# Performance work log

Measured on AMD Instinct MI355X. Metric: run time of the kernel, lower is better.

## Reference

```python
import jax, jax.numpy as jnp
import numpy as np

B, IN_DIM, HID, OUT_DIM = 32768, 784, 256, 1000
L, CURV = 3, 1e-3
LOG2_H = 8  # log2(HID)
EPS_BN = 1e-5

def _layer_param_sizes():
    return [(HID // (2 * (1 << (l % LOG2_H)))) * 2 for l in range(L)]

def setup_inputs():
    key = jax.random.key(0)
    ks = jax.random.split(key, 4)
    total = sum(_layer_param_sizes())  # 448
    return {
        "x": jax.random.normal(ks[0], (B, IN_DIM), jnp.float32),
        "fc1_w": jax.random.normal(ks[1], (HID, IN_DIM), jnp.float32) / np.sqrt(IN_DIM).astype(np.float32),
        "fc1_b": jnp.zeros((HID,), jnp.float32),
        "bn1_gamma": jnp.ones((HID,), jnp.float32),
        "bn1_beta": jnp.zeros((HID,), jnp.float32),
        "bf_params": jax.random.normal(ks[2], (total,), jnp.float32) * 0.01,
        "bn2_gamma": jnp.ones((HID,), jnp.float32),
        "bn2_beta": jnp.zeros((HID,), jnp.float32),
        "fc2_w": jax.random.normal(ks[3], (OUT_DIM, HID), jnp.float32) / np.sqrt(HID).astype(np.float32),
        "fc2_b": jnp.zeros((OUT_DIM,), jnp.float32),
    }

def _batchnorm(h, gamma, beta):
    # training-mode BatchNorm1d: batch mean / biased variance
    mu = jnp.mean(h, axis=0)
    var = jnp.mean(jnp.square(h - mu), axis=0)
    return gamma * (h - mu) * jax.lax.rsqrt(var + EPS_BN) + beta

def _log_map0(x, c):
    # Poincare ball log map at origin: artanh(sqrt(c)|x|) * x / (sqrt(c)|x|)
    sn = jnp.sqrt(c) * jnp.linalg.norm(x, axis=-1, keepdims=True)
    sn = jnp.clip(sn, 1e-7, 1.0 - 1e-6)
    return (jnp.arctanh(sn) / sn) * x

def _exp_map0(u, c):
    sn = jnp.maximum(jnp.sqrt(c) * jnp.linalg.norm(u, axis=-1, keepdims=True), 1e-7)
    return (jnp.tanh(sn) / sn) * u

def _hyper_butterfly(h, params, c):
    u = _log_map0(h, c)
    off = 0
    for l in range(L):
        bs = 1 << (l % LOG2_H)      # half-block size at stage l
        nb = HID // (2 * bs)        # number of 2x2-rotation blocks
        p = params[off:off + 2 * nb]
        a = p[:nb][None, :, None]   # [1, nb, 1]
        b = p[nb:][None, :, None]
        v = u.reshape(-1, nb, 2, bs)
        x1, x2 = v[:, :, 0], v[:, :, 1]
        y1 = a * x1 + b * x2
        y2 = -b * x1 + a * x2
        u = jnp.stack([y1, y2], axis=2).reshape(-1, HID)
        off += 2 * nb
    return _exp_map0(u, c)

def reference(x, fc1_w, fc1_b, bn1_gamma, bn1_beta, bf_params, bn2_gamma, bn2_beta, fc2_w, fc2_b):
    h = x @ fc1_w.T + fc1_b
    h = jax.nn.relu(_batchnorm(h, bn1_gamma, bn1_beta))
    ht = _hyper_butterfly(h, bf_params, CURV)
    ht = jax.nn.relu(_batchnorm(ht, bn2_gamma, bn2_beta))
    return ht @ fc2_w.T + fc2_b
```

## Files before the change

kernel.cpp:

```cpp
#include <hip/hip_runtime.h>
#include <math.h>

#define NBATCH 32768
#define IND    784
#define KPAD1  800
#define HIDD   256
#define OUTD   1000
#define OUTDP  1024

typedef _Float16 half8  __attribute__((ext_vector_type(8)));
typedef _Float16 half4v __attribute__((ext_vector_type(4)));
typedef float    floatx4 __attribute__((ext_vector_type(4)));

#define GAS __attribute__((address_space(1)))
#define LAS __attribute__((address_space(3)))

#define WAITVM_BAR(N)                                                      \
    asm volatile("s_waitcnt vmcnt(" #N ") lgkmcnt(0)" ::: "memory");       \
    __builtin_amdgcn_s_barrier();                                          \
    __builtin_amdgcn_sched_barrier(0)

__device__ __forceinline__ void gld16(const void* g, void* l) {
    __builtin_amdgcn_global_load_lds((const GAS void*)g, (LAS void*)l, 16, 0, 0);
}

__device__ __forceinline__ float wave_allreduce_sum(float v) {
    #pragma unroll
    for (int off = 32; off >= 1; off >>= 1) v += __shfl_xor(v, off);
    return v;
}

__global__ __launch_bounds__(256)
void prep_kernel(const float* __restrict__ w1, _Float16* __restrict__ w1h,
                 const float* __restrict__ w2, _Float16* __restrict__ w2h,
                 float* __restrict__ stat)
{
    const int tid = threadIdx.x;
    if (blockIdx.x == 0) {
        for (int j = tid; j < 1024 + 16; j += 256) stat[j] = 0.0f;
    }
    const int NW1 = HIDD * (KPAD1 / 8);
    const int NW2 = OUTDP * (HIDD / 8);
    for (int i = blockIdx.x * 256 + tid; i < NW1 + NW2; i += (int)gridDim.x * 256) {
        half8 o;
        if (i < NW1) {
            const int r = i / (KPAD1 / 8), c8 = (i % (KPAD1 / 8)) * 8;
            if (c8 + 8 <= IND) {
                const float* s = &w1[(size_t)r * IND + c8];
                float4 v0 = *(const float4*)s, v1 = *(const float4*)(s + 4);
                o[0]=(_Float16)v0.x; o[1]=(_Float16)v0.y; o[2]=(_Float16)v0.z; o[3]=(_Float16)v0.w;
                o[4]=(_Float16)v1.x; o[5]=(_Float16)v1.y; o[6]=(_Float16)v1.z; o[7]=(_Float16)v1.w;
            } else {
                #pragma unroll
                for (int j = 0; j < 8; ++j) o[j] = (_Float16)0.0f;
            }
            *(half8*)&w1h[(size_t)r * KPAD1 + c8] = o;
        } else {
            const int k = i - NW1;
            const int r = k >> 5, c8 = (k & 31) * 8;
            if (r < OUTD) {
                const float* s = &w2[(size_t)r * HIDD + c8];
                float4 v0 = *(const float4*)s, v1 = *(const float4*)(s + 4);
                o[0]=(_Float16)v0.x; o[1]=(_Float16)v0.y; o[2]=(_Float16)v0.z; o[3]=(_Float16)v0.w;
                o[4]=(_Float16)v1.x; o[5]=(_Float16)v1.y; o[6]=(_Float16)v1.z; o[7]=(_Float16)v1.w;
            } else {
                #pragma unroll
                for (int j = 0; j < 8; ++j) o[j] = (_Float16)0.0f;
            }
            *(half8*)&w2h[(size_t)r * HIDD + c8] = o;
        }
    }
}

__global__ __launch_bounds__(256, 2)
void gemm1_kernel(const float* __restrict__ x, const _Float16* __restrict__ w1h,
                  const float* __restrict__ b1, const float* __restrict__ zbuf,
                  float* __restrict__ h, float* __restrict__ sum1, float* __restrict__ ssq1)
{
    __shared__ __align__(16) float    ldsA[3][4096];
    __shared__ __align__(16) _Float16 ldsB[3][4096];
    __shared__ float redS[2][128], redQ[2][128];

    const int tid  = threadIdx.x;
    const int bid0 = blockIdx.x;
    const int vbid = (bid0 & 7) * 64 + (bid0 >> 3);
    const int bm = vbid >> 1, bn = vbid & 1;
    const int m0 = bm * 128, n0 = bn * 128;
    const int lane = tid & 63, wv = tid >> 6;
    const int wr = wv >> 1, wc = wv & 1;
    const int l15 = lane & 15, lg = lane >> 4;
    const int e7 = l15 & 7, e3 = l15 & 3;
    const int nt = KPAD1 / 32;

    const int arow = lane >> 3, agp = (lane & 7) ^ arow;
    const int brow = lane >> 2, bgp = (lane & 3) ^ (brow & 3);
    const float*    Ab = x   + (size_t)(m0 + arow) * IND   + agp * 4;
    const _Float16* Bb = w1h + (size_t)(n0 + brow) * KPAD1 + bgp * 8;

    floatx4 acc[4][4];
    #pragma unroll
    for (int i = 0; i < 4; ++i)
        #pragma unroll
        for (int j = 0; j < 4; ++j) acc[i][j] = (floatx4){0.f, 0.f, 0.f, 0.f};

    auto STAGE = [&](int buf, int t) {
        const int t32 = t * 32;
        const bool tok = t < nt;
        const bool aok = tok && (t32 + agp * 4) < IND;
        #pragma unroll
        for (int c = 0; c < 4; ++c) {
            const int ch = wv + c * 4;
            const float* s = aok ? (Ab + (size_t)ch * 8 * IND + t32) : zbuf;
            gld16(s, &ldsA[buf][ch * 256]);
        }
        #pragma unroll
        for (int c = 0; c < 2; ++c) {
            const int ch = wv + c * 4;
            const void* s = tok ? (const void*)(Bb + (size_t)ch * 16 * KPAD1 + t32)
                                : (const void*)zbuf;
            gld16(s, &ldsB[buf][ch * 512]);
        }
    };

    STAGE(0, 0);
    STAGE(1, 1);
    WAITVM_BAR(6);

    int buf = 0;
    for (int t = 0; t < nt; ++t) {
        int nbuf = buf + 2; if (nbuf >= 3) nbuf -= 3;
        STAGE(nbuf, t + 2);
        half8 af[4], bfr[4];
        #pragma unroll
        for (int i = 0; i < 4; ++i) {
            const int rc = wr * 8 + i * 2 + (l15 >> 3);
            const float* base = &ldsA[buf][rc * 256 + e7 * 32];
            float4 va = *(const float4*)(base + (((2 * lg)     ^ e7) * 4));
            float4 vb = *(const float4*)(base + (((2 * lg + 1) ^ e7) * 4));
            half8 hv;
            hv[0]=(_Float16)va.x; hv[1]=(_Float16)va.y; hv[2]=(_Float16)va.z; hv[3]=(_Float16)va.w;
            hv[4]=(_Float16)vb.x; hv[5]=(_Float16)vb.y; hv[6]=(_Float16)vb.z; hv[7]=(_Float16)vb.w;
            af[i] = hv;
        }
        #pragma unroll
        for (int j = 0; j < 4; ++j)
            bfr[j] = *(const half8*)&ldsB[buf][(wc * 4 + j) * 512 + l15 * 32 + ((lg ^ e3) * 8)];
        #pragma unroll
        for (int i = 0; i < 4; ++i)
            #pragma unroll
            for (int j = 0; j < 4; ++j)
                acc[i][j] = __builtin_amdgcn_mfma_f32_16x16x32_f16(bfr[j], af[i], acc[i][j], 0, 0, 0);
        WAITVM_BAR(6);
        buf = (buf + 1 == 3) ? 0 : buf + 1;
    }

    float sJ[4][4], qJ[4][4];
    #pragma unroll
    for (int j = 0; j < 4; ++j)
        #pragma unroll
        for (int r = 0; r < 4; ++r) { sJ[j][r] = 0.f; qJ[j][r] = 0.f; }
    #pragma unroll
    for (int i = 0; i < 4; ++i) {
        const int m = m0 + wr * 64 + i * 16 + l15;
        #pragma unroll
        for (int j = 0; j < 4; ++j) {
            const int nb = n0 + wc * 64 + j * 16 + lg * 4;
            float4 bt = *reinterpret_cast<const float4*>(&b1[nb]);
            float v[4] = {acc[i][j][0] + bt.x, acc[i][j][1] + bt.y,
                          acc[i][j][2] + bt.z, acc[i][j][3] + bt.w};
            *reinterpret_cast<float4*>(&h[(size_t)m * HIDD + nb]) =
                make_float4(v[0], v[1], v[2], v[3]);
            #pragma unroll
            for (int r = 0; r < 4; ++r) { sJ[j][r] += v[r]; qJ[j][r] += v[r] * v[r]; }
        }
    }
    #pragma unroll
    for (int j = 0; j < 4; ++j)
        #pragma unroll
        for (int r = 0; r < 4; ++r) {
            float s = sJ[j][r], q = qJ[j][r];
            s += __shfl_xor(s, 1); s += __shfl_xor(s, 2);
            s += __shfl_xor(s, 4); s += __shfl_xor(s, 8);
            q += __shfl_xor(q, 1); q += __shfl_xor(q, 2);
            q += __shfl_xor(q, 4); q += __shfl_xor(q, 8);
            if (l15 == 0) {
                redS[wr][wc * 64 + j * 16 + lg * 4 + r] = s;
                redQ[wr][wc * 64 + j * 16 + lg * 4 + r] = q;
            }
        }
    __syncthreads();
    if (tid < 128) {
        atomicAdd(&sum1[n0 + tid], redS[0][tid] + redS[1][tid]);
        atomicAdd(&ssq1[n0 + tid], redQ[0][tid] + redQ[1][tid]);
    }
}

__global__ __launch_bounds__(256)
void mid_kernel(const float* __restrict__ h, const float* __restrict__ bfp,
                const float* __restrict__ sum1, const float* __restrict__ ssq1,
                const float* __restrict__ g1, const float* __restrict__ be1,
                _Float16* __restrict__ ht16, float* __restrict__ sum2, float* __restrict__ ssq2)
{
    __shared__ float s1sh[256], t1sh[256];
    __shared__ float bsum[4][256], bssq[4][256];
    const int tid  = threadIdx.x;
    {
        const float inv = 1.0f / (float)NBATCH;
        const float mu  = sum1[tid] * inv;
        const float var = fmaxf(ssq1[tid] * inv - mu * mu, 0.0f);
        const float rs  = 1.0f / sqrtf(var + 1e-5f);
        const float sj  = g1[tid] * rs;
        s1sh[tid] = sj;
        t1sh[tid] = fmaf(-mu, sj, be1[tid]);
    }
    __syncthreads();

    const int w    = tid >> 6;
    const int lane = tid & 63;
    const int row0 = blockIdx.x * 64 + w * 16;
    const int c0   = lane * 4;

    const float4 s1v = *reinterpret_cast<const float4*>(&s1sh[c0]);
    const float4 t1v = *reinterpret_cast<const float4*>(&t1sh[c0]);
    const float a0 = bfp[2 * lane],       a1 = bfp[2 * lane + 1];
    const float b0 = bfp[128 + 2 * lane], b1 = bfp[128 + 2 * lane + 1];
    const float a2 = bfp[256 + lane],     b2 = bfp[320 + lane];
    const float a3 = bfp[384 + (lane >> 1)], b3 = bfp[416 + (lane >> 1)];
    const float sgn = (lane & 1) ? -1.0f : 1.0f;
    const float sc  = sqrtf(1e-3f);

    float ps0 = 0, ps1 = 0, ps2 = 0, ps3 = 0;
    float q0 = 0, q1 = 0, q2 = 0, q3 = 0;

    for (int r = 0; r < 16; ++r) {
        const int row = row0 + r;
        const float4 v = *reinterpret_cast<const float4*>(&h[(size_t)row * HIDD + c0]);
        float x0 = fmaxf(fmaf(v.x, s1v.x, t1v.x), 0.0f);
        float x1 = fmaxf(fmaf(v.y, s1v.y, t1v.y), 0.0f);
        float x2 = fmaxf(fmaf(v.z, s1v.z, t1v.z), 0.0f);
        float x3 = fmaxf(fmaf(v.w, s1v.w, t1v.w), 0.0f);
        float n2 = x0 * x0 + x1 * x1 + x2 * x2 + x3 * x3;
        n2 = wave_allreduce_sum(n2);
        float sn = sc * sqrtf(n2);
        sn = fminf(fmaxf(sn, 1e-7f), 1.0f - 1e-6f);
        const float ls = atanhf(sn) / sn;
        x0 *= ls; x1 *= ls; x2 *= ls; x3 *= ls;
        const float y0 = fmaf(a0, x0,  b0 * x1);
        const float y1 = fmaf(a0, x1, -b0 * x0);
        const float y2 = fmaf(a1, x2,  b1 * x3);
        const float y3 = fmaf(a1, x3, -b1 * x2);
        const float z0 = fmaf(a2, y0,  b2 * y2);
        const float z1 = fmaf(a2, y1,  b2 * y3);
        const float z2 = fmaf(a2, y2, -b2 * y0);
        const float z3 = fmaf(a2, y3, -b2 * y1);
        const float p0 = __shfl_xor(z0, 1);
        const float p1 = __shfl_xor(z1, 1);
        const float p2 = __shfl_xor(z2, 1);
        const float p3 = __shfl_xor(z3, 1);
        const float w0 = fmaf(a3, z0, sgn * (b3 * p0));
        const float w1 = fmaf(a3, z1, sgn * (b3 * p1));
        const float w2 = fmaf(a3, z2, sgn * (b3 * p2));
        const float w3 = fmaf(a3, z3, sgn * (b3 * p3));
        float m2 = w0 * w0 + w1 * w1 + w2 * w2 + w3 * w3;
        m2 = wave_allreduce_sum(m2);
        const float sn2 = fmaxf(sc * sqrtf(m2), 1e-7f);
        const float es = tanhf(sn2) / sn2;
        const float o0 = es * w0, o1 = es * w1, o2 = es * w2, o3 = es * w3;
        half4v hv;
        hv[0] = (_Float16)(o0 * 65536.0f); hv[1] = (_Float16)(o1 * 65536.0f);
        hv[2] = (_Float16)(o2 * 65536.0f); hv[3] = (_Float16)(o3 * 65536.0f);
        *reinterpret_cast<half4v*>(&ht16[(size_t)row * HIDD + c0]) = hv;
        ps0 += o0; ps1 += o1; ps2 += o2; ps3 += o3;
        q0 += o0 * o0; q1 += o1 * o1; q2 += o2 * o2; q3 += o3 * o3;
    }

    bsum[w][c0 + 0] = ps0; bsum[w][c0 + 1] = ps1; bsum[w][c0 + 2] = ps2; bsum[w][c0 + 3] = ps3;
    bssq[w][c0 + 0] = q0;  bssq[w][c0 + 1] = q1;  bssq[w][c0 + 2] = q2;  bssq[w][c0 + 3] = q3;
    __syncthreads();
    if (tid < 256) {
        const float s = bsum[0][tid] + bsum[1][tid] + bsum[2][tid] + bsum[3][tid];
        const float q = bssq[0][tid] + bssq[1][tid] + bssq[2][tid] + bssq[3][tid];
        atomicAdd(&sum2[tid], s);
        atomicAdd(&ssq2[tid], q);
    }
}

__global__ __launch_bounds__(256, 3)
void gemm2_kernel(const _Float16* __restrict__ ht16, const _Float16* __restrict__ w2h,
                  const float* __restrict__ b2,
                  const float* __restrict__ sum2, const float* __restrict__ ssq2,
                  const float* __restrict__ g2, const float* __restrict__ be2,
                  const float* __restrict__ zbuf, float* __restrict__ out)
{
    __shared__ __align__(16) _Float16 ldsA[3][4096];
    __shared__ __align__(16) _Float16 ldsB[3][4096];
    __shared__ float sf[256], tf[256];

    const int tid = threadIdx.x;
    {
        const float inv = 1.0f / (float)NBATCH;
        const float mu  = sum2[tid] * inv;
        const float var = fmaxf(ssq2[tid] * inv - mu * mu, 0.0f);
        const float rs  = 1.0f / sqrtf(var + 1e-5f);
        const float sj  = g2[tid] * rs;
        sf[tid] = sj * (1024.0f / 65536.0f);
        tf[tid] = fmaf(-mu, sj, be2[tid]) * 1024.0f;
    }

    const int bid0 = blockIdx.x;
    const int vbid = (bid0 & 7) * 256 + (bid0 >> 3);
    const int bm = vbid >> 3, bn = vbid & 7;
    const int m0 = bm * 128, n0 = bn * 128;
    const int lane = tid & 63, wv = tid >> 6;
    const int wr = wv >> 1, wc = wv & 1;
    const int l15 = lane & 15, lg = lane >> 4;
    const int e3 = l15 & 3;
    const int nt = HIDD / 32;

    const int srow = lane >> 2, sgp = (lane & 3) ^ (srow & 3);
    const _Float16* Ab = ht16 + (size_t)(m0 + srow) * HIDD + sgp * 8;
    const _Float16* Bb = w2h  + (size_t)(n0 + srow) * HIDD + sgp * 8;

    floatx4 acc[4][4];
    #pragma unroll
    for (int i = 0; i < 4; ++i)
        #pragma unroll
        for (int j = 0; j < 4; ++j) acc[i][j] = (floatx4){0.f, 0.f, 0.f, 0.f};

    auto STAGE = [&](int buf, int t) {
        const int t32 = t * 32;
        const bool tok = t < nt;
        #pragma unroll
        for (int c = 0; c < 2; ++c) {
            const int ch = wv + c * 4;
            const void* sa = tok ? (const void*)(Ab + (size_t)ch * 16 * HIDD + t32)
                                 : (const void*)zbuf;
            const void* sb = tok ? (const void*)(Bb + (size_t)ch * 16 * HIDD + t32)
                                 : (const void*)zbuf;
            gld16(sa, &ldsA[buf][ch * 512]);
            gld16(sb, &ldsB[buf][ch * 512]);
        }
    };

    STAGE(0, 0);
    STAGE(1, 1);
    WAITVM_BAR(4);

    int buf = 0;
    for (int t = 0; t < nt; ++t) {
        int nbuf = buf + 2; if (nbuf >= 3) nbuf -= 3;
        STAGE(nbuf, t + 2);
        const int kb = t * 32 + lg * 8;
        float4 s0 = *(const float4*)&sf[kb], s1 = *(const float4*)&sf[kb + 4];
        float4 t0 = *(const float4*)&tf[kb], t1 = *(const float4*)&tf[kb + 4];
        half8 af[4], bfr[4];
        #pragma unroll
        for (int i = 0; i < 4; ++i) {
            half8 v = *(const half8*)&ldsA[buf][(wr * 4 + i) * 512 + l15 * 32 + ((lg ^ e3) * 8)];
            half8 hv;
            hv[0] = (_Float16)fmaxf(fmaf((float)v[0], s0.x, t0.x), 0.0f);
            hv[1] = (_Float16)fmaxf(fmaf((float)v[1], s0.y, t0.y), 0.0f);
            hv[2] = (_Float16)fmaxf(fmaf((float)v[2], s0.z, t0.z), 0.0f);
            hv[3] = (_Float16)fmaxf(fmaf((float)v[3], s0.w, t0.w), 0.0f);
            hv[4] = (_Float16)fmaxf(fmaf((float)v[4], s1.x, t1.x), 0.0f);
            hv[5] = (_Float16)fmaxf(fmaf((float)v[5], s1.y, t1.y), 0.0f);
            hv[6] = (_Float16)fmaxf(fmaf((float)v[6], s1.z, t1.z), 0.0f);
            hv[7] = (_Float16)fmaxf(fmaf((float)v[7], s1.w, t1.w), 0.0f);
            af[i] = hv;
        }
        #pragma unroll
        for (int j = 0; j < 4; ++j)
            bfr[j] = *(const half8*)&ldsB[buf][(wc * 4 + j) * 512 + l15 * 32 + ((lg ^ e3) * 8)];
        #pragma unroll
        for (int i = 0; i < 4; ++i)
            #pragma unroll
            for (int j = 0; j < 4; ++j)
                acc[i][j] = __builtin_amdgcn_mfma_f32_16x16x32_f16(bfr[j], af[i], acc[i][j], 0, 0, 0);
        WAITVM_BAR(4);
        buf = (buf + 1 == 3) ? 0 : buf + 1;
    }
    asm volatile("s_waitcnt vmcnt(0)" ::: "memory");

    const float invScale = 1.0f / 1024.0f;
    #pragma unroll
    for (int i = 0; i < 4; ++i) {
        const int m = m0 + wr * 64 + i * 16 + l15;
        #pragma unroll
        for (int j = 0; j < 4; ++j) {
            const int nb = n0 + wc * 64 + j * 16 + lg * 4;
            float bj[4];
            if (nb + 4 <= OUTD) {
                float4 bt = *reinterpret_cast<const float4*>(&b2[nb]);
                bj[0] = bt.x; bj[1] = bt.y; bj[2] = bt.z; bj[3] = bt.w;
            } else {
                #pragma unroll
                for (int r = 0; r < 4; ++r) bj[r] = (nb + r < OUTD) ? b2[nb + r] : 0.0f;
            }
            float v[4];
            #pragma unroll
            for (int r = 0; r < 4; ++r) v[r] = fmaf(acc[i][j][r], invScale, bj[r]);
            if (nb + 4 <= OUTD) {
                *reinterpret_cast<float4*>(&out[(size_t)m * OUTD + nb]) =
                    make_float4(v[0], v[1], v[2], v[3]);
            } else {
                #pragma unroll
                for (int r = 0; r < 4; ++r)
                    if (nb + r < OUTD) out[(size_t)m * OUTD + nb + r] = v[r];
            }
        }
    }
}

extern "C" void kernel_launch(void* const* d_in, const int* in_sizes, int n_in,
                              void* d_out, int out_size, void* d_ws, size_t ws_size,
                              hipStream_t stream)
{
    const float* x   = (const float*)d_in[0];
    const float* w1  = (const float*)d_in[1];
    const float* b1  = (const float*)d_in[2];
    const float* g1  = (const float*)d_in[3];
    const float* be1 = (const float*)d_in[4];
    const float* bfp = (const float*)d_in[5];
    const float* g2  = (const float*)d_in[6];
    const float* be2 = (const float*)d_in[7];
    const float* w2  = (const float*)d_in[8];
    const float* b2  = (const float*)d_in[9];

    float* out = (float*)d_out;
    char*  wsb = (char*)d_ws;

    _Float16* ht16 = (_Float16*)(wsb);
    _Float16* w1h  = (_Float16*)(wsb + 16777216);
    _Float16* w2h  = (_Float16*)(wsb + 17186816);
    float*    stat = (float*)  (wsb + 17711104);
    float* sum1 = stat;
    float* ssq1 = stat + 256;
    float* sum2 = stat + 512;
    float* ssq2 = stat + 768;
    float* zbuf = stat + 1024;

    float* h = out;

    prep_kernel<<<232, 256, 0, stream>>>(w1, w1h, w2, w2h, stat);
    gemm1_kernel<<<512, 256, 0, stream>>>(x, w1h, b1, zbuf, h, sum1, ssq1);
    mid_kernel<<<512, 256, 0, stream>>>(h, bfp, sum1, ssq1, g1, be1, ht16, sum2, ssq2);
    gemm2_kernel<<<2048, 256, 0, stream>>>(ht16, w2h, b2, sum2, ssq2, g2, be2, zbuf, out);
}
```

Before: 129.4 us.

## Stage gemm1 A tiles via registers as fp16 to cut LDS and raise occupancy

The first GEMM now loads x tiles from global memory into registers, converts them to fp16, and writes them to a double-buffered fp16 LDS buffer. Previously it DMA'd fp32 data straight into a triple-buffered LDS area and converted on every fragment read. This halves LDS use for A, which allows launch bounds of three blocks per CU instead of two, and removes repeated conversions on the read side. In exchange it adds register pressure for the staged loads, a more complex two-phase unrolled loop with explicit vmcnt waits, and global-load latency that must be hidden by the register prefetch.

```diff
diff --git a/kernel.cpp b/kernel.cpp
--- a/kernel.cpp
+++ b/kernel.cpp
@@ -15,6 +15,7 @@
 #define GAS __attribute__((address_space(1)))
 #define LAS __attribute__((address_space(3)))
 
+#define WAITVM(N) asm volatile("s_waitcnt vmcnt(" #N ")" ::: "memory")
 #define WAITVM_BAR(N)                                                      \
     asm volatile("s_waitcnt vmcnt(" #N ") lgkmcnt(0)" ::: "memory");       \
     __builtin_amdgcn_s_barrier();                                          \
@@ -72,12 +73,12 @@
     }
 }
 
-__global__ __launch_bounds__(256, 2)
+__global__ __launch_bounds__(256, 3)
 void gemm1_kernel(const float* __restrict__ x, const _Float16* __restrict__ w1h,
                   const float* __restrict__ b1, const float* __restrict__ zbuf,
                   float* __restrict__ h, float* __restrict__ sum1, float* __restrict__ ssq1)
 {
-    __shared__ __align__(16) float    ldsA[3][4096];
+    __shared__ __align__(16) _Float16 ldsA[2][4096];
     __shared__ __align__(16) _Float16 ldsB[3][4096];
     __shared__ float redS[2][128], redQ[2][128];
 
@@ -89,12 +90,18 @@
     const int lane = tid & 63, wv = tid >> 6;
     const int wr = wv >> 1, wc = wv & 1;
     const int l15 = lane & 15, lg = lane >> 4;
-    const int e7 = l15 & 7, e3 = l15 & 3;
+    const int e3 = l15 & 3;
     const int nt = KPAD1 / 32;
 
-    const int arow = lane >> 3, agp = (lane & 7) ^ arow;
+    const int r0g = tid >> 2;
+    const int r1g = 64 + (tid >> 2);
+    const int kq  = tid & 3;
+    const int wpos0 = r0g * 32 + ((kq ^ (r0g & 3)) * 8);
+    const int wpos1 = r1g * 32 + ((kq ^ (r1g & 3)) * 8);
+    const float* Ab0 = x + (size_t)(m0 + r0g) * IND + kq * 8;
+    const float* Ab1 = x + (size_t)(m0 + r1g) * IND + kq * 8;
+
     const int brow = lane >> 2, bgp = (lane & 3) ^ (brow & 3);
-    const float*    Ab = x   + (size_t)(m0 + arow) * IND   + agp * 4;
     const _Float16* Bb = w1h + (size_t)(n0 + brow) * KPAD1 + bgp * 8;
 
     floatx4 acc[4][4];
@@ -103,56 +110,84 @@
         #pragma unroll
         for (int j = 0; j < 4; ++j) acc[i][j] = (floatx4){0.f, 0.f, 0.f, 0.f};
 
-    auto STAGE = [&](int buf, int t) {
+    floatx4 rgaE[4], rgaO[4];
+
+    auto A_ISSUE = [&](floatx4 (&rg)[4], int t) {
+        const int t32 = t * 32;
+        const bool v = (t32 + kq * 8) < IND;
+        const float* p0 = v ? (Ab0 + t32) : zbuf;
+        const float* p1 = v ? (Ab1 + t32) : zbuf;
+        rg[0] = *(const floatx4*)p0;
+        rg[1] = *(const floatx4*)(p0 + 4);
+        rg[2] = *(const floatx4*)p1;
+        rg[3] = *(const floatx4*)(p1 + 4);
+    };
+    auto A_WRITE = [&](floatx4 (&rg)[4], int wb) {
+        half8 h0, h1;
+        #pragma unroll
+        for (int j = 0; j < 4; ++j) {
+            h0[j] = (_Float16)rg[0][j]; h0[4 + j] = (_Float16)rg[1][j];
+            h1[j] = (_Float16)rg[2][j]; h1[4 + j] = (_Float16)rg[3][j];
+        }
+        *(half8*)&ldsA[wb][wpos0] = h0;
+        *(half8*)&ldsA[wb][wpos1] = h1;
+    };
+    auto B_ISSUE = [&](int bb, int t) {
         const int t32 = t * 32;
         const bool tok = t < nt;
-        const bool aok = tok && (t32 + agp * 4) < IND;
-        #pragma unroll
-        for (int c = 0; c < 4; ++c) {
-            const int ch = wv + c * 4;
-            const float* s = aok ? (Ab + (size_t)ch * 8 * IND + t32) : zbuf;
-            gld16(s, &ldsA[buf][ch * 256]);
-        }
         #pragma unroll
         for (int c = 0; c < 2; ++c) {
             const int ch = wv + c * 4;
             const void* s = tok ? (const void*)(Bb + (size_t)ch * 16 * KPAD1 + t32)
                                 : (const void*)zbuf;
-            gld16(s, &ldsB[buf][ch * 512]);
+            gld16(s, &ldsB[bb][ch * 512]);
         }
     };
 
-    STAGE(0, 0);
-    STAGE(1, 1);
-    WAITVM_BAR(6);
-
-    int buf = 0;
-    for (int t = 0; t < nt; ++t) {
-        int nbuf = buf + 2; if (nbuf >= 3) nbuf -= 3;
-        STAGE(nbuf, t + 2);
+    auto COMPUTE = [&](int abuf, int brd) {
         half8 af[4], bfr[4];
         #pragma unroll
-        for (int i = 0; i < 4; ++i) {
-            const int rc = wr * 8 + i * 2 + (l15 >> 3);
-            const float* base = &ldsA[buf][rc * 256 + e7 * 32];
-            float4 va = *(const float4*)(base + (((2 * lg)     ^ e7) * 4));
-            float4 vb = *(const float4*)(base + (((2 * lg + 1) ^ e7) * 4));
-            half8 hv;
-            hv[0]=(_Float16)va.x; hv[1]=(_Float16)va.y; hv[2]=(_Float16)va.z; hv[3]=(_Float16)va.w;
-            hv[4]=(_Float16)vb.x; hv[5]=(_Float16)vb.y; hv[6]=(_Float16)vb.z; hv[7]=(_Float16)vb.w;
-            af[i] = hv;
-        }
+        for (int i = 0; i < 4; ++i)
+            af[i] = *(const half8*)&ldsA[abuf][(wr * 64 + i * 16 + l15) * 32 + ((lg ^ e3) * 8)];
         #pragma unroll
         for (int j = 0; j < 4; ++j)
-            bfr[j] = *(const half8*)&ldsB[buf][(wc * 4 + j) * 512 + l15 * 32 + ((lg ^ e3) * 8)];
+            bfr[j] = *(const half8*)&ldsB[brd][(wc * 4 + j) * 512 + l15 * 32 + ((lg ^ e3) * 8)];
         #pragma unroll
         for (int i = 0; i < 4; ++i)
             #pragma unroll
             for (int j = 0; j < 4; ++j)
                 acc[i][j] = __builtin_amdgcn_mfma_f32_16x16x32_f16(bfr[j], af[i], acc[i][j], 0, 0, 0);
+    };
+
+    A_ISSUE(rgaE, 0); B_ISSUE(0, 0);
+    WAITVM(2);
+    A_WRITE(rgaE, 0);
+    A_ISSUE(rgaO, 1); B_ISSUE(1, 1);
+    WAITVM_BAR(6);
+
+    int b0 = 0;
+    for (int p = 0; p < 12; ++p) {
+        const int t  = p * 2;
+        const int b1v = b0 + 1 == 3 ? 0 : b0 + 1;
+        const int b2v = b1v + 1 == 3 ? 0 : b1v + 1;
+        A_ISSUE(rgaE, t + 2);
+        B_ISSUE(b2v, t + 2);
+        COMPUTE(0, b0);
+        __builtin_amdgcn_sched_barrier(0);
+        WAITVM(6);
+        A_WRITE(rgaO, 1);
         WAITVM_BAR(6);
-        buf = (buf + 1 == 3) ? 0 : buf + 1;
-    }
+        A_ISSUE(rgaO, t + 3);
+        B_ISSUE(b0, t + 3);
+        COMPUTE(1, b1v);
+        __builtin_amdgcn_sched_barrier(0);
+        WAITVM(6);
+        A_WRITE(rgaE, 0);
+        WAITVM_BAR(6);
+        b0 = b2v;
+    }
+    COMPUTE(0, b0);
+    WAITVM(0);
 
     float sJ[4][4], qJ[4][4];
     #pragma unroll
@@ -379,7 +414,7 @@
         WAITVM_BAR(4);
         buf = (buf + 1 == 3) ? 0 : buf + 1;
     }
-    asm volatile("s_waitcnt vmcnt(0)" ::: "memory");
+    WAITVM(0);
 
     const float invScale = 1.0f / 1024.0f;
     #pragma unroll
```

Result: faster. 126.4 us (-2.3%).

## Restructure gemm1 to full-N tiles with register-direct A loads

Applied to the files above, without the earlier changes.

gemm1 now has each 512-thread block compute a 128x256 tile, i.e. all of N, so each row of x is read once instead of twice. The A operand is loaded straight from global memory into registers per wave, bypassing LDS, while B is staged through LDS in five phases of 160 K. The aim is to halve x traffic and drop the A LDS round trip. The cost is more registers (16 accumulators plus 5 staged A fragments), 256 blocks at one block per CU, and coarser phase barriers with less overlap between loads and MFMA.

```diff
diff --git a/kernel.cpp b/kernel.cpp
--- a/kernel.cpp
+++ b/kernel.cpp
@@ -15,8 +15,13 @@
 #define GAS __attribute__((address_space(1)))
 #define LAS __attribute__((address_space(3)))
 
+#define WAITVM(N) asm volatile("s_waitcnt vmcnt(" #N ")" ::: "memory")
 #define WAITVM_BAR(N)                                                      \
     asm volatile("s_waitcnt vmcnt(" #N ") lgkmcnt(0)" ::: "memory");       \
+    __builtin_amdgcn_s_barrier();                                          \
+    __builtin_amdgcn_sched_barrier(0)
+#define LGKM_BAR                                                           \
+    asm volatile("s_waitcnt lgkmcnt(0)" ::: "memory");                     \
     __builtin_amdgcn_s_barrier();                                          \
     __builtin_amdgcn_sched_barrier(0)
 
@@ -72,126 +77,98 @@
     }
 }
 
-__global__ __launch_bounds__(256, 2)
+__global__ __launch_bounds__(512, 1)
 void gemm1_kernel(const float* __restrict__ x, const _Float16* __restrict__ w1h,
                   const float* __restrict__ b1, const float* __restrict__ zbuf,
                   float* __restrict__ h, float* __restrict__ sum1, float* __restrict__ ssq1)
 {
-    __shared__ __align__(16) float    ldsA[3][4096];
-    __shared__ __align__(16) _Float16 ldsB[3][4096];
-    __shared__ float redS[2][128], redQ[2][128];
+    __shared__ __align__(16) _Float16 ldsB[5][16][512];
+    __shared__ float redS[8][256], redQ[8][256];
 
     const int tid  = threadIdx.x;
-    const int bid0 = blockIdx.x;
-    const int vbid = (bid0 & 7) * 64 + (bid0 >> 3);
-    const int bm = vbid >> 1, bn = vbid & 1;
-    const int m0 = bm * 128, n0 = bn * 128;
-    const int lane = tid & 63, wv = tid >> 6;
-    const int wr = wv >> 1, wc = wv & 1;
-    const int l15 = lane & 15, lg = lane >> 4;
-    const int e7 = l15 & 7, e3 = l15 & 3;
-    const int nt = KPAD1 / 32;
-
-    const int arow = lane >> 3, agp = (lane & 7) ^ arow;
-    const int brow = lane >> 2, bgp = (lane & 3) ^ (brow & 3);
-    const float*    Ab = x   + (size_t)(m0 + arow) * IND   + agp * 4;
-    const _Float16* Bb = w1h + (size_t)(n0 + brow) * KPAD1 + bgp * 8;
-
-    floatx4 acc[4][4];
-    #pragma unroll
-    for (int i = 0; i < 4; ++i)
-        #pragma unroll
-        for (int j = 0; j < 4; ++j) acc[i][j] = (floatx4){0.f, 0.f, 0.f, 0.f};
-
-    auto STAGE = [&](int buf, int t) {
-        const int t32 = t * 32;
-        const bool tok = t < nt;
-        const bool aok = tok && (t32 + agp * 4) < IND;
-        #pragma unroll
-        for (int c = 0; c < 4; ++c) {
-            const int ch = wv + c * 4;
-            const float* s = aok ? (Ab + (size_t)ch * 8 * IND + t32) : zbuf;
-            gld16(s, &ldsA[buf][ch * 256]);
-        }
-        #pragma unroll
-        for (int c = 0; c < 2; ++c) {
-            const int ch = wv + c * 4;
-            const void* s = tok ? (const void*)(Bb + (size_t)ch * 16 * KPAD1 + t32)
-                                : (const void*)zbuf;
-            gld16(s, &ldsB[buf][ch * 512]);
-        }
+    const int w    = tid >> 6;
+    const int lane = tid & 63;
+    const int l15  = lane & 15, lg = lane >> 4;
+    const int m0   = (int)blockIdx.x * 128;
+    const int mrow = m0 + w * 16 + l15;
+
+    const int bri = lane >> 2;
+    const int bgp = (lane & 3) ^ (bri & 3);
+    const float* aptr = x + (size_t)mrow * IND;
+
+    floatx4 acc[16];
+    #pragma unroll
+    for (int j = 0; j < 16; ++j) acc[j] = (floatx4){0.f, 0.f, 0.f, 0.f};
+
+    floatx4 a0[2], a1[2], a2[2], a3[2], a4[2];
+
+    auto A_ISSUE = [&](floatx4 (&st)[2], int kt) {
+        const int col = kt * 32 + lg * 8;
+        const float* p = (col < IND) ? (aptr + col) : zbuf;
+        st[0] = *(const floatx4*)p;
+        st[1] = *(const floatx4*)(p + 4);
     };
-
-    STAGE(0, 0);
-    STAGE(1, 1);
-    WAITVM_BAR(6);
-
-    int buf = 0;
-    for (int t = 0; t < nt; ++t) {
-        int nbuf = buf + 2; if (nbuf >= 3) nbuf -= 3;
-        STAGE(nbuf, t + 2);
-        half8 af[4], bfr[4];
-        #pragma unroll
-        for (int i = 0; i < 4; ++i) {
-            const int rc = wr * 8 + i * 2 + (l15 >> 3);
-            const float* base = &ldsA[buf][rc * 256 + e7 * 32];
-            float4 va = *(const float4*)(base + (((2 * lg)     ^ e7) * 4));
-            float4 vb = *(const float4*)(base + (((2 * lg + 1) ^ e7) * 4));
-            half8 hv;
-            hv[0]=(_Float16)va.x; hv[1]=(_Float16)va.y; hv[2]=(_Float16)va.z; hv[3]=(_Float16)va.w;
-            hv[4]=(_Float16)vb.x; hv[5]=(_Float16)vb.y; hv[6]=(_Float16)vb.z; hv[7]=(_Float16)vb.w;
-            af[i] = hv;
-        }
-        #pragma unroll
-        for (int j = 0; j < 4; ++j)
-            bfr[j] = *(const half8*)&ldsB[buf][(wc * 4 + j) * 512 + l15 * 32 + ((lg ^ e3) * 8)];
-        #pragma unroll
-        for (int i = 0; i < 4; ++i)
+    auto B_STAGE = [&](int p) {
+        #pragma unroll
+        for (int ks = 0; ks < 5; ++ks)
             #pragma unroll
-            for (int j = 0; j < 4; ++j)
-                acc[i][j] = __builtin_amdgcn_mfma_f32_16x16x32_f16(bfr[j], af[i], acc[i][j], 0, 0, 0);
-        WAITVM_BAR(6);
-        buf = (buf + 1 == 3) ? 0 : buf + 1;
-    }
-
-    float sJ[4][4], qJ[4][4];
-    #pragma unroll
-    for (int j = 0; j < 4; ++j)
-        #pragma unroll
-        for (int r = 0; r < 4; ++r) { sJ[j][r] = 0.f; qJ[j][r] = 0.f; }
-    #pragma unroll
-    for (int i = 0; i < 4; ++i) {
-        const int m = m0 + wr * 64 + i * 16 + l15;
-        #pragma unroll
-        for (int j = 0; j < 4; ++j) {
-            const int nb = n0 + wc * 64 + j * 16 + lg * 4;
-            float4 bt = *reinterpret_cast<const float4*>(&b1[nb]);
-            float v[4] = {acc[i][j][0] + bt.x, acc[i][j][1] + bt.y,
-                          acc[i][j][2] + bt.z, acc[i][j][3] + bt.w};
-            *reinterpret_cast<float4*>(&h[(size_t)m * HIDD + nb]) =
-                make_float4(v[0], v[1], v[2], v[3]);
-            #pragma unroll
-            for (int r = 0; r < 4; ++r) { sJ[j][r] += v[r]; qJ[j][r] += v[r] * v[r]; }
-        }
-    }
-    #pragma unroll
-    for (int j = 0; j < 4; ++j)
+            for (int c = 0; c < 2; ++c) {
+                const int ch = w * 2 + c;
+                const _Float16* src = w1h + (size_t)(ch * 16 + bri) * KPAD1
+                                      + p * 160 + ks * 32 + bgp * 8;
+                gld16(src, &ldsB[ks][ch][lane * 8]);
+            }
+    };
+    auto STEP = [&](floatx4 (&st)[2], int ks) {
+        half8 af;
+        #pragma unroll
+        for (int q = 0; q < 4; ++q) { af[q] = (_Float16)st[0][q]; af[4+q] = (_Float16)st[1][q]; }
+        const int ro = l15 * 32 + ((lg ^ (l15 & 3)) * 8);
+        #pragma unroll
+        for (int j = 0; j < 16; ++j) {
+            half8 bf = *(const half8*)&ldsB[ks][j][ro];
+            acc[j] = __builtin_amdgcn_mfma_f32_16x16x32_f16(bf, af, acc[j], 0, 0, 0);
+        }
+    };
+
+    #pragma unroll
+    for (int p = 0; p < 5; ++p) {
+        if (p > 0) { LGKM_BAR; }
+        B_STAGE(p);
+        A_ISSUE(a0, 5*p+0); A_ISSUE(a1, 5*p+1); A_ISSUE(a2, 5*p+2);
+        A_ISSUE(a3, 5*p+3); A_ISSUE(a4, 5*p+4);
+        WAITVM_BAR(10);
+        STEP(a0, 0); STEP(a1, 1); STEP(a2, 2); STEP(a3, 3); STEP(a4, 4);
+    }
+
+    #pragma unroll
+    for (int j = 0; j < 16; ++j) {
+        const int nb = j * 16 + lg * 4;
+        float4 bt = *reinterpret_cast<const float4*>(&b1[nb]);
+        float v[4] = {acc[j][0] + bt.x, acc[j][1] + bt.y,
+                      acc[j][2] + bt.z, acc[j][3] + bt.w};
+        *reinterpret_cast<float4*>(&h[(size_t)mrow * HIDD + nb]) =
+            make_float4(v[0], v[1], v[2], v[3]);
         #pragma unroll
         for (int r = 0; r < 4; ++r) {
-            float s = sJ[j][r], q = qJ[j][r];
+            float s = v[r], q = v[r] * v[r];
             s += __shfl_xor(s, 1); s += __shfl_xor(s, 2);
             s += __shfl_xor(s, 4); s += __shfl_xor(s, 8);
             q += __shfl_xor(q, 1); q += __shfl_xor(q, 2);
             q += __shfl_xor(q, 4); q += __shfl_xor(q, 8);
             if (l15 == 0) {
-                redS[wr][wc * 64 + j * 16 + lg * 4 + r] = s;
-                redQ[wr][wc * 64 + j * 16 + lg * 4 + r] = q;
-            }
-        }
+                redS[w][nb + r] = s;
+                redQ[w][nb + r] = q;
+            }
+        }
+    }
     __syncthreads();
-    if (tid < 128) {
-        atomicAdd(&sum1[n0 + tid], redS[0][tid] + redS[1][tid]);
-        atomicAdd(&ssq1[n0 + tid], redQ[0][tid] + redQ[1][tid]);
+    if (tid < 256) {
+        float s = 0.f, q = 0.f;
+        #pragma unroll
+        for (int ww = 0; ww < 8; ++ww) { s += redS[ww][tid]; q += redQ[ww][tid]; }
+        atomicAdd(&sum1[tid], s);
+        atomicAdd(&ssq1[tid], q);
     }
 }
 
@@ -379,7 +356,7 @@
         WAITVM_BAR(4);
         buf = (buf + 1 == 3) ? 0 : buf + 1;
     }
-    asm volatile("s_waitcnt vmcnt(0)" ::: "memory");
+    WAITVM(0);
 
     const float invScale = 1.0f / 1024.0f;
     #pragma unroll
@@ -442,7 +419,7 @@
     float* h = out;
 
     prep_kernel<<<232, 256, 0, stream>>>(w1, w1h, w2, w2h, stat);
-    gemm1_kernel<<<512, 256, 0, stream>>>(x, w1h, b1, zbuf, h, sum1, ssq1);
+    gemm1_kernel<<<256, 512, 0, stream>>>(x, w1h, b1, zbuf, h, sum1, ssq1);
     mid_kernel<<<512, 256, 0, stream>>>(h, bfp, sum1, ssq1, g1, be1, ht16, sum2, ssq2);
     gemm2_kernel<<<2048, 256, 0, stream>>>(ht16, w2h, b2, sum2, ssq2, g2, be2, zbuf, out);
 }
```

Result: slower. 140.1 us (+8.3%).

## Pre-convert x to padded fp16 in separate kernel before first GEMM

Applied to the files above, without the earlier changes.

A new kernel converts the fp32 input x into a zero-padded fp16 buffer (stride 800), stored in unused space of the output buffer. gemm1 then stages A tiles as fp16 through the same swizzled LDS path as the weights. This halves gemm1's A-tile LDS footprint, removes the per-iteration fp32-to-fp16 conversions, and raises launch bounds to 3 blocks per CU. The trade-off is an extra kernel launch and an extra round trip through global memory: x is read as fp32, written as fp16, then read again.

```diff
diff --git a/kernel.cpp b/kernel.cpp
--- a/kernel.cpp
+++ b/kernel.cpp
@@ -15,6 +15,7 @@
 #define GAS __attribute__((address_space(1)))
 #define LAS __attribute__((address_space(3)))
 
+#define WAITVM(N) asm volatile("s_waitcnt vmcnt(" #N ")" ::: "memory")
 #define WAITVM_BAR(N)                                                      \
     asm volatile("s_waitcnt vmcnt(" #N ") lgkmcnt(0)" ::: "memory");       \
     __builtin_amdgcn_s_barrier();                                          \
@@ -28,6 +29,28 @@
     #pragma unroll
     for (int off = 32; off >= 1; off >>= 1) v += __shfl_xor(v, off);
     return v;
+}
+
+__global__ __launch_bounds__(256)
+void cvt_x_kernel(const float* __restrict__ x, _Float16* __restrict__ x16)
+{
+    const unsigned NG = NBATCH * 100u;
+    for (unsigned i = blockIdx.x * 256u + threadIdx.x; i < NG;
+         i += (unsigned)gridDim.x * 256u) {
+        const unsigned row = i / 100u;
+        const unsigned g   = i - row * 100u;
+        half8 o;
+        if (g < 98u) {
+            const float* s = &x[(size_t)row * IND + g * 8u];
+            float4 v0 = *(const float4*)s, v1 = *(const float4*)(s + 4);
+            o[0]=(_Float16)v0.x; o[1]=(_Float16)v0.y; o[2]=(_Float16)v0.z; o[3]=(_Float16)v0.w;
+            o[4]=(_Float16)v1.x; o[5]=(_Float16)v1.y; o[6]=(_Float16)v1.z; o[7]=(_Float16)v1.w;
+        } else {
+            #pragma unroll
+            for (int j = 0; j < 8; ++j) o[j] = (_Float16)0.0f;
+        }
+        *(half8*)&x16[(size_t)row * KPAD1 + g * 8u] = o;
+    }
 }
 
 __global__ __launch_bounds__(256)
@@ -72,12 +95,12 @@
     }
 }
 
-__global__ __launch_bounds__(256, 2)
-void gemm1_kernel(const float* __restrict__ x, const _Float16* __restrict__ w1h,
+__global__ __launch_bounds__(256, 3)
+void gemm1_kernel(const _Float16* __restrict__ x16, const _Float16* __restrict__ w1h,
                   const float* __restrict__ b1, const float* __restrict__ zbuf,
                   float* __restrict__ h, float* __restrict__ sum1, float* __restrict__ ssq1)
 {
-    __shared__ __align__(16) float    ldsA[3][4096];
+    __shared__ __align__(16) _Float16 ldsA[3][4096];
     __shared__ __align__(16) _Float16 ldsB[3][4096];
     __shared__ float redS[2][128], redQ[2][128];
 
@@ -89,13 +112,12 @@
     const int lane = tid & 63, wv = tid >> 6;
     const int wr = wv >> 1, wc = wv & 1;
     const int l15 = lane & 15, lg = lane >> 4;
-    const int e7 = l15 & 7, e3 = l15 & 3;
+    const int e3 = l15 & 3;
     const int nt = KPAD1 / 32;
 
-    const int arow = lane >> 3, agp = (lane & 7) ^ arow;
-    const int brow = lane >> 2, bgp = (lane & 3) ^ (brow & 3);
-    const float*    Ab = x   + (size_t)(m0 + arow) * IND   + agp * 4;
-    const _Float16* Bb = w1h + (size_t)(n0 + brow) * KPAD1 + bgp * 8;
+    const int srow = lane >> 2, sgp = (lane & 3) ^ (srow & 3);
+    const _Float16* Ab = x16 + (size_t)(m0 + srow) * KPAD1 + sgp * 8;
+    const _Float16* Bb = w1h + (size_t)(n0 + srow) * KPAD1 + sgp * 8;
 
     floatx4 acc[4][4];
     #pragma unroll
@@ -106,25 +128,21 @@
     auto STAGE = [&](int buf, int t) {
         const int t32 = t * 32;
         const bool tok = t < nt;
-        const bool aok = tok && (t32 + agp * 4) < IND;
-        #pragma unroll
-        for (int c = 0; c < 4; ++c) {
-            const int ch = wv + c * 4;
-            const float* s = aok ? (Ab + (size_t)ch * 8 * IND + t32) : zbuf;
-            gld16(s, &ldsA[buf][ch * 256]);
-        }
         #pragma unroll
         for (int c = 0; c < 2; ++c) {
             const int ch = wv + c * 4;
-            const void* s = tok ? (const void*)(Bb + (size_t)ch * 16 * KPAD1 + t32)
-                                : (const void*)zbuf;
-            gld16(s, &ldsB[buf][ch * 512]);
+            const void* sa = tok ? (const void*)(Ab + (size_t)ch * 16 * KPAD1 + t32)
+                                 : (const void*)zbuf;
+            const void* sb = tok ? (const void*)(Bb + (size_t)ch * 16 * KPAD1 + t32)
+                                 : (const void*)zbuf;
+            gld16(sa, &ldsA[buf][ch * 512]);
+            gld16(sb, &ldsB[buf][ch * 512]);
         }
     };
 
     STAGE(0, 0);
     STAGE(1, 1);
-    WAITVM_BAR(6);
+    WAITVM_BAR(4);
 
     int buf = 0;
     for (int t = 0; t < nt; ++t) {
@@ -132,16 +150,8 @@
         STAGE(nbuf, t + 2);
         half8 af[4], bfr[4];
         #pragma unroll
-        for (int i = 0; i < 4; ++i) {
-            const int rc = wr * 8 + i * 2 + (l15 >> 3);
-            const float* base = &ldsA[buf][rc * 256 + e7 * 32];
-            float4 va = *(const float4*)(base + (((2 * lg)     ^ e7) * 4));
-            float4 vb = *(const float4*)(base + (((2 * lg + 1) ^ e7) * 4));
-            half8 hv;
-            hv[0]=(_Float16)va.x; hv[1]=(_Float16)va.y; hv[2]=(_Float16)va.z; hv[3]=(_Float16)va.w;
-            hv[4]=(_Float16)vb.x; hv[5]=(_Float16)vb.y; hv[6]=(_Float16)vb.z; hv[7]=(_Float16)vb.w;
-            af[i] = hv;
-        }
+        for (int i = 0; i < 4; ++i)
+            af[i] = *(const half8*)&ldsA[buf][(wr * 4 + i) * 512 + l15 * 32 + ((lg ^ e3) * 8)];
         #pragma unroll
         for (int j = 0; j < 4; ++j)
             bfr[j] = *(const half8*)&ldsB[buf][(wc * 4 + j) * 512 + l15 * 32 + ((lg ^ e3) * 8)];
@@ -150,9 +160,10 @@
             #pragma unroll
             for (int j = 0; j < 4; ++j)
                 acc[i][j] = __builtin_amdgcn_mfma_f32_16x16x32_f16(bfr[j], af[i], acc[i][j], 0, 0, 0);
-        WAITVM_BAR(6);
+        WAITVM_BAR(4);
         buf = (buf + 1 == 3) ? 0 : buf + 1;
     }
+    WAITVM(0);
 
     float sJ[4][4], qJ[4][4];
     #pragma unroll
@@ -379,7 +390,7 @@
         WAITVM_BAR(4);
         buf = (buf + 1 == 3) ? 0 : buf + 1;
     }
-    asm volatile("s_waitcnt vmcnt(0)" ::: "memory");
+    WAITVM(0);
 
     const float invScale = 1.0f / 1024.0f;
     #pragma unroll
@@ -439,10 +450,12 @@
     float* ssq2 = stat + 768;
     float* zbuf = stat + 1024;
 
-    float* h = out;
-
+    float*    h   = out;
+    _Float16* x16 = (_Float16*)(out + 8388608);
+
+    cvt_x_kernel<<<2048, 256, 0, stream>>>(x, x16);
     prep_kernel<<<232, 256, 0, stream>>>(w1, w1h, w2, w2h, stat);
-    gemm1_kernel<<<512, 256, 0, stream>>>(x, w1h, b1, zbuf, h, sum1, ssq1);
+    gemm1_kernel<<<512, 256, 0, stream>>>(x16, w1h, b1, zbuf, h, sum1, ssq1);
     mid_kernel<<<512, 256, 0, stream>>>(h, bfp, sum1, ssq1, g1, be1, ht16, sum2, ssq2);
     gemm2_kernel<<<2048, 256, 0, stream>>>(ht16, w2h, b2, sum2, ssq2, g2, be2, zbuf, out);
 }
```

Measured after the change: 145.6 us. 1.13x slower.
